# Kernel tuning notes

Hardware: AMD Instinct MI355X
Metric: run time of the kernel (lower is better)

Reference implementation:

```python
import jax, jax.numpy as jnp
import numpy as np

N, E = 16000, 256000
IN_DIM, HID, OUT_DIM, NH = 128, 128, 128, 16
HD = OUT_DIM // NH  # 8
EDGE_F, R_F = 4, 20
KV_IN = 2 * IN_DIM + EDGE_F + R_F  # 280
EPS = 1e-5
INV_SQRT_HD = float(1.0 / np.sqrt(HD))


def _ln(x, g, b):
    mu = jnp.mean(x, -1, keepdims=True)
    var = jnp.mean(jnp.square(x - mu), -1, keepdims=True)
    return (x - mu) * jax.lax.rsqrt(var + EPS) * g + b


def _mlp(x, W1, b1, g, be, W2, b2):
    # Linear -> LayerNorm -> ReLU -> Linear (targetdiff-style 2-layer MLP)
    hdn = jax.nn.relu(_ln(x @ W1 + b1, g, be))
    return hdn @ W2 + b2


def setup_inputs() -> dict:
    key = jax.random.key(0)
    k = jax.random.split(key, 16)
    s = 0.02
    f32 = jnp.float32
    return {
        "h": jax.random.normal(k[0], (N, IN_DIM), f32),
        "rel_x": jax.random.normal(k[1], (E, 3), f32),
        "r_feat": jax.random.uniform(k[2], (E, R_F), f32),
        "edge_feat": jax.random.normal(k[3], (E, EDGE_F), f32),
        "edge_index": jax.random.randint(k[4], (2, E), 0, N),
        # xk MLP: KV_IN -> HID -> OUT_DIM
        "xk_W1": jax.random.normal(k[5], (KV_IN, HID), f32) * s,
        "xk_b1": jnp.zeros((HID,), f32),
        "xk_g": jnp.ones((HID,), f32),
        "xk_be": jnp.zeros((HID,), f32),
        "xk_W2": jax.random.normal(k[6], (HID, OUT_DIM), f32) * s,
        "xk_b2": jnp.zeros((OUT_DIM,), f32),
        # xv MLP: KV_IN -> HID -> NH
        "xv_W1": jax.random.normal(k[7], (KV_IN, HID), f32) * s,
        "xv_b1": jnp.zeros((HID,), f32),
        "xv_g": jnp.ones((HID,), f32),
        "xv_be": jnp.zeros((HID,), f32),
        "xv_W2": jax.random.normal(k[8], (HID, NH), f32) * s,
        "xv_b2": jnp.zeros((NH,), f32),
        # xq MLP: IN_DIM -> HID -> OUT_DIM
        "xq_W1": jax.random.normal(k[9], (IN_DIM, HID), f32) * s,
        "xq_b1": jnp.zeros((HID,), f32),
        "xq_g": jnp.ones((HID,), f32),
        "xq_be": jnp.zeros((HID,), f32),
        "xq_W2": jax.random.normal(k[10], (HID, OUT_DIM), f32) * s,
        "xq_b2": jnp.zeros((OUT_DIM,), f32),
        # ew_net: Linear(R_F, 1) + sigmoid
        "ew_W": jax.random.normal(k[11], (R_F, 1), f32) * s,
        "ew_b": jnp.zeros((1,), f32),
    }


def reference(h, rel_x, r_feat, edge_feat, edge_index,
              xk_W1, xk_b1, xk_g, xk_be, xk_W2, xk_b2,
              xv_W1, xv_b1, xv_g, xv_be, xv_W2, xv_b2,
              xq_W1, xq_b1, xq_g, xq_be, xq_W2, xq_b2,
              ew_W, ew_b):
    n = h.shape[0]
    src, dst = edge_index[0], edge_index[1]
    hi, hj = h[dst], h[src]                                    # [E, IN_DIM] each
    kv_input = jnp.concatenate([edge_feat, r_feat, hi, hj], -1)  # [E, KV_IN]
    k = _mlp(kv_input, xk_W1, xk_b1, xk_g, xk_be, xk_W2, xk_b2).reshape(-1, NH, HD)
    v = _mlp(kv_input, xv_W1, xv_b1, xv_g, xv_be, xv_W2, xv_b2)  # [E, NH]
    e_w = jax.nn.sigmoid(r_feat @ ew_W + ew_b)                   # [E, 1]
    v = v * e_w
    v = v[:, :, None] * rel_x[:, None, :]                        # [E, NH, 3]
    q = _mlp(h, xq_W1, xq_b1, xq_g, xq_be, xq_W2, xq_b2).reshape(-1, NH, HD)
    scores = jnp.sum(q[dst] * k, -1) * INV_SQRT_HD               # [E, NH]
    # scatter_softmax over dst groups (numerically stable)
    smax = jax.lax.stop_gradient(jax.ops.segment_max(scores, dst, num_segments=n))
    ex = jnp.exp(scores - smax[dst])
    denom = jax.ops.segment_sum(ex, dst, num_segments=n)
    alpha = ex / denom[dst]                                      # [E, NH]
    m = alpha[:, :, None] * v                                    # [E, NH, 3]
    out = jax.ops.segment_sum(m, dst, num_segments=n)            # [N, NH, 3]
    return out.mean(1)                                           # [N, 3]
```

## Files before the change

kernel.cpp:

```cpp
#include <hip/hip_runtime.h>
#include <math.h>

#define NN 16000
#define NE 256000
#define INV_SQRT_HD 0.35355339059327373f
#define LN_EPS 1e-5f

typedef __attribute__((ext_vector_type(8))) short bf16x8;
typedef __attribute__((ext_vector_type(4))) float f32x4;

__device__ inline unsigned short f2bf(float x) {
    unsigned u = __float_as_uint(x);
    unsigned r = ((u >> 16) & 1u) + 0x7FFFu;
    return (unsigned short)((u + r) >> 16);
}

__global__ __launch_bounds__(256) void prep_kernel(
    const float* __restrict__ h,
    const float* __restrict__ r_feat,
    const float* __restrict__ edge_feat,
    const float* __restrict__ ewW, const float* __restrict__ ewB,
    const float* __restrict__ kW1, const float* __restrict__ vW1,
    const float* __restrict__ kW2, const float* __restrict__ vW2,
    const float* __restrict__ qW1, const float* __restrict__ qW2,
    unsigned short* __restrict__ h_bf, unsigned short* __restrict__ feats_bf,
    float* __restrict__ ew_pre,
    unsigned short* __restrict__ w1p, unsigned short* __restrict__ w2p,
    unsigned short* __restrict__ w1q, unsigned short* __restrict__ w2q)
{
    const int b = blockIdx.x, t = threadIdx.x;
    if (b < 1000) {
        const int gid = b * 256 + t;
        const float4* hp = (const float4*)(h + (size_t)gid * 8);
        float4 a = hp[0], c = hp[1];
        ushort4 u0, u1;
        u0.x = f2bf(a.x); u0.y = f2bf(a.y); u0.z = f2bf(a.z); u0.w = f2bf(a.w);
        u1.x = f2bf(c.x); u1.y = f2bf(c.y); u1.z = f2bf(c.z); u1.w = f2bf(c.w);
        *(ushort4*)(h_bf + (size_t)gid * 8) = u0;
        *(ushort4*)(h_bf + (size_t)gid * 8 + 4) = u1;
    } else if (b < 2000) {
        const int e = (b - 1000) * 256 + t;
        float4 ef = *(const float4*)(edge_feat + (size_t)e * 4);
        float rf[20];
        #pragma unroll
        for (int i = 0; i < 5; ++i)
            *(float4*)&rf[i * 4] = *(const float4*)(r_feat + (size_t)e * 20 + i * 4);
        float z = ewB[0];
        #pragma unroll
        for (int i = 0; i < 20; ++i) z = fmaf(rf[i], ewW[i], z);
        ew_pre[e] = (1.f / (1.f + expf(-z))) * (1.f / 16.f);
        unsigned short fb[32];
        fb[0] = f2bf(ef.x); fb[1] = f2bf(ef.y); fb[2] = f2bf(ef.z); fb[3] = f2bf(ef.w);
        #pragma unroll
        for (int i = 0; i < 20; ++i) fb[4 + i] = f2bf(rf[i]);
        #pragma unroll
        for (int i = 24; i < 32; ++i) fb[i] = 0;
        #pragma unroll
        for (int i = 0; i < 4; ++i)
            *(int4*)(feats_bf + (size_t)e * 32 + i * 8) = *(int4*)&fb[i * 8];
    } else {
        const int idx = (b - 2000) * 256 + t;
        if (idx < 73728) {
            int j = idx & 7, l = (idx >> 3) & 63, mtc = (idx >> 9) & 15, s = idx >> 13;
            int kp = s * 32 + (l >> 4) * 8 + j;
            int col = mtc * 16 + (l & 15);
            float v = 0.f;
            int row = (kp < 24) ? kp : ((kp >= 32) ? (kp - 8) : -1);
            if (row >= 0) v = (col < 128) ? kW1[(size_t)row * 128 + col]
                                          : vW1[(size_t)row * 128 + col - 128];
            w1p[idx] = f2bf(v);
        } else if (idx < 92160) {
            int i2 = idx - 73728;
            int j = i2 & 7, l = (i2 >> 3) & 63, sc = i2 >> 9;
            int ct = sc % 9, s2 = sc / 9;
            int k = s2 * 32 + (l >> 4) * 8 + j;
            float v = (ct < 8) ? kW2[(size_t)k * 128 + ct * 16 + (l & 15)]
                               : vW2[(size_t)k * 16 + (l & 15)];
            w2p[i2] = f2bf(v);
        } else if (idx < 108544) {
            int i3 = idx - 92160;
            int j = i3 & 7, l = (i3 >> 3) & 63, mt = (i3 >> 9) & 7, s = i3 >> 12;
            int k = s * 32 + (l >> 4) * 8 + j;
            w1q[i3] = f2bf(qW1[(size_t)k * 128 + mt * 16 + (l & 15)]);
        } else if (idx < 124928) {
            int i4 = idx - 108544;
            int j = i4 & 7, l = (i4 >> 3) & 63, mt = (i4 >> 9) & 7, s = i4 >> 12;
            int k = s * 32 + (l >> 4) * 8 + j;
            w2q[i4] = f2bf(qW2[(size_t)k * 128 + mt * 16 + (l & 15)]);
        }
    }
}

__global__ __launch_bounds__(256, 4) void qmlp_kernel(
    const unsigned short* __restrict__ h_bf,
    const float* __restrict__ B1, const float* __restrict__ G,
    const float* __restrict__ BE, const float* __restrict__ B2,
    const unsigned short* __restrict__ w1q, const unsigned short* __restrict__ w2q,
    float* __restrict__ qout)
{
    __shared__ __align__(16) unsigned char hsq[8192];
    __shared__ float2 lnb[4][32];
    __shared__ float  gb1[128];
    __shared__ float2 gbe[128];
    __shared__ float  gb2[128];

    const int t = threadIdx.x;
    const int nb = blockIdx.x * 32;
    const int wc = t >> 6, l = t & 63, lrow = l & 15, lgrp = l >> 4;

    if (t < 128) { gb1[t] = B1[t]; gbe[t] = make_float2(G[t], BE[t]); gb2[t] = B2[t]; }

    unsigned offN[2];
    #pragma unroll
    for (int nt = 0; nt < 2; ++nt)
        offN[nt] = (unsigned)(nb + nt * 16 + lrow) * 128 + lgrp * 8;
    __syncthreads();

    f32x4 acc1[2][2];
    #pragma unroll
    for (int mt = 0; mt < 2; ++mt) {
        const int cb = wc * 32 + mt * 16 + lgrp * 4;
        #pragma unroll
        for (int nt = 0; nt < 2; ++nt) {
            acc1[mt][nt][0] = gb1[cb];     acc1[mt][nt][1] = gb1[cb + 1];
            acc1[mt][nt][2] = gb1[cb + 2]; acc1[mt][nt][3] = gb1[cb + 3];
        }
    }
    {
        auto ldA = [&](int s, bf16x8* dst) {
            #pragma unroll
            for (int mt = 0; mt < 2; ++mt)
                dst[mt] = *(const bf16x8*)(w1q + (size_t)((s * 8 + wc * 2 + mt) * 64 + l) * 8);
        };
        auto ldB = [&](int s, bf16x8* dst) {
            #pragma unroll
            for (int nt = 0; nt < 2; ++nt)
                dst[nt] = *(const bf16x8*)(h_bf + offN[nt] + s * 32);
        };
        bf16x8 aB[2][2], bB[2][2];
        ldA(0, aB[0]); ldB(0, bB[0]);
        ldA(1, aB[1]); ldB(1, bB[1]);
        #pragma unroll
        for (int s = 0; s < 4; ++s) {
            const int c = s & 1;
            #pragma unroll
            for (int mt = 0; mt < 2; ++mt)
                #pragma unroll
                for (int nt = 0; nt < 2; ++nt)
                    acc1[mt][nt] = __builtin_amdgcn_mfma_f32_16x16x32_bf16(aB[c][mt], bB[c][nt], acc1[mt][nt], 0, 0, 0);
            if (s < 2) { ldA(s + 2, aB[c]); ldB(s + 2, bB[c]); }
        }
    }

    float2 myln[2];
    #pragma unroll
    for (int nt = 0; nt < 2; ++nt) {
        float p1 = 0.f, p2 = 0.f;
        #pragma unroll
        for (int mt = 0; mt < 2; ++mt)
            #pragma unroll
            for (int r = 0; r < 4; ++r) { float v = acc1[mt][nt][r]; p1 += v; p2 += v * v; }
        p1 += __shfl_xor(p1, 16); p2 += __shfl_xor(p2, 16);
        p1 += __shfl_xor(p1, 32); p2 += __shfl_xor(p2, 32);
        myln[nt] = make_float2(p1, p2);
        if (l < 16) lnb[wc][nt * 16 + l] = myln[nt];
    }
    __syncthreads();

    #pragma unroll
    for (int nt = 0; nt < 2; ++nt) {
        const int el = nt * 16 + lrow;
        float2 a0 = lnb[0][el], a1 = lnb[1][el], a2 = lnb[2][el], a3 = lnb[3][el];
        const float s1 = a0.x + a1.x + a2.x + a3.x;
        const float s2 = a0.y + a1.y + a2.y + a3.y;
        const float mu = s1 * (1.f / 128.f);
        const float rs = rsqrtf(s2 * (1.f / 128.f) - mu * mu + LN_EPS);
        #pragma unroll
        for (int mt = 0; mt < 2; ++mt) {
            const int cb = wc * 32 + mt * 16 + lgrp * 4;
            const float2 g0 = gbe[cb], g1 = gbe[cb+1], g2 = gbe[cb+2], g3 = gbe[cb+3];
            ushort4 u;
            u.x = f2bf(fmaxf((acc1[mt][nt][0] - mu) * rs * g0.x + g0.y, 0.f));
            u.y = f2bf(fmaxf((acc1[mt][nt][1] - mu) * rs * g1.x + g1.y, 0.f));
            u.z = f2bf(fmaxf((acc1[mt][nt][2] - mu) * rs * g2.x + g2.y, 0.f));
            u.w = f2bf(fmaxf((acc1[mt][nt][3] - mu) * rs * g3.x + g3.y, 0.f));
            *(ushort4*)(hsq + ((cb >> 3) * 32 + el) * 16 + (lgrp & 1) * 8) = u;
        }
    }
    __syncthreads();

    f32x4 acc2[2][2];
    #pragma unroll
    for (int km = 0; km < 2; ++km) {
        const int c2 = (wc * 2 + km) * 16 + lgrp * 4;
        #pragma unroll
        for (int nt = 0; nt < 2; ++nt) {
            acc2[km][nt][0] = gb2[c2];     acc2[km][nt][1] = gb2[c2 + 1];
            acc2[km][nt][2] = gb2[c2 + 2]; acc2[km][nt][3] = gb2[c2 + 3];
        }
    }
    {
        bf16x8 a0C = *(const bf16x8*)(w2q + (size_t)((wc * 2) * 64 + l) * 8);
        bf16x8 a1C = *(const bf16x8*)(w2q + (size_t)((wc * 2 + 1) * 64 + l) * 8);
        #pragma unroll
        for (int s2 = 0; s2 < 4; ++s2) {
            bf16x8 a0N, a1N;
            if (s2 < 3) {
                a0N = *(const bf16x8*)(w2q + (size_t)(((s2+1) * 8 + wc * 2) * 64 + l) * 8);
                a1N = *(const bf16x8*)(w2q + (size_t)(((s2+1) * 8 + wc * 2 + 1) * 64 + l) * 8);
            }
            bf16x8 hb[2];
            #pragma unroll
            for (int nt = 0; nt < 2; ++nt)
                hb[nt] = *(const bf16x8*)(hsq + (((s2 * 4 + lgrp) * 32) + nt * 16 + lrow) * 16);
            #pragma unroll
            for (int nt = 0; nt < 2; ++nt) {
                acc2[0][nt] = __builtin_amdgcn_mfma_f32_16x16x32_bf16(a0C, hb[nt], acc2[0][nt], 0, 0, 0);
                acc2[1][nt] = __builtin_amdgcn_mfma_f32_16x16x32_bf16(a1C, hb[nt], acc2[1][nt], 0, 0, 0);
            }
            a0C = a0N; a1C = a1N;
        }
    }
    #pragma unroll
    for (int km = 0; km < 2; ++km) {
        const int c2 = (wc * 2 + km) * 16 + lgrp * 4;
        #pragma unroll
        for (int nt = 0; nt < 2; ++nt) {
            const int el = nt * 16 + lrow;
            float4 o;
            o.x = acc2[km][nt][0]; o.y = acc2[km][nt][1];
            o.z = acc2[km][nt][2]; o.w = acc2[km][nt][3];
            *(float4*)(qout + (size_t)(nb + el) * 128 + c2) = o;
        }
    }
}

__global__ __launch_bounds__(256, 4) void edge_kernel(
    const unsigned short* __restrict__ h_bf,
    const unsigned short* __restrict__ feats_bf,
    const int*   __restrict__ eidx,
    const float* __restrict__ ew_pre,
    const float* __restrict__ kB1, const float* __restrict__ kG, const float* __restrict__ kBE,
    const float* __restrict__ vB1, const float* __restrict__ vG, const float* __restrict__ vBE,
    const float* __restrict__ kB2, const float* __restrict__ vB2,
    const unsigned short* __restrict__ w1p, const unsigned short* __restrict__ w2p,
    const float* __restrict__ q,
    float* __restrict__ ex_out, float* __restrict__ vw_out, float* __restrict__ denom)
{
    __shared__ __align__(16) unsigned char hs[16384];
    __shared__ float2 lnb[4][32];
    __shared__ float  gb1[256];
    __shared__ float2 gbe[256];
    __shared__ float  gb2[144];
    __shared__ int    dst_sh[32];
    __shared__ float  ew_s[32];

    const int t = threadIdx.x;
    const int eb = blockIdx.x * 32;
    const int wc = t >> 6, l = t & 63, lrow = l & 15, lgrp = l >> 4;

    gb1[t] = (t < 128) ? kB1[t] : vB1[t - 128];
    gbe[t] = make_float2((t < 128) ? kG[t] : vG[t - 128],
                         (t < 128) ? kBE[t] : vBE[t - 128]);
    if (t < 144) gb2[t] = (t < 128) ? kB2[t] : vB2[t - 128];
    if (t < 32) {
        dst_sh[t] = eidx[NE + eb + t];
        ew_s[t]   = ew_pre[eb + t];
    }

    unsigned offF[2], offD[2], offS[2];
    #pragma unroll
    for (int nt = 0; nt < 2; ++nt) {
        const int e = eb + nt * 16 + lrow;
        offF[nt] = (unsigned)e * 32 + lgrp * 8;
        offD[nt] = (unsigned)eidx[NE + e] * 128 + lgrp * 8;
        offS[nt] = (unsigned)eidx[e] * 128 + lgrp * 8;
    }
    __syncthreads();

    f32x4 acc1[4][2];
    #pragma unroll
    for (int mt = 0; mt < 4; ++mt) {
        const int cb = wc * 64 + mt * 16 + lgrp * 4;
        #pragma unroll
        for (int nt = 0; nt < 2; ++nt) {
            acc1[mt][nt][0] = gb1[cb];     acc1[mt][nt][1] = gb1[cb + 1];
            acc1[mt][nt][2] = gb1[cb + 2]; acc1[mt][nt][3] = gb1[cb + 3];
        }
    }
    {
        auto ldA = [&](int s, bf16x8* dst) {
            #pragma unroll
            for (int mt = 0; mt < 4; ++mt)
                dst[mt] = *(const bf16x8*)(w1p + (size_t)((s * 16 + wc * 4 + mt) * 64 + l) * 8);
        };
        auto ldB = [&](int s, bf16x8* dst) {
            #pragma unroll
            for (int nt = 0; nt < 2; ++nt) {
                const unsigned short* p = (s == 0) ? (feats_bf + offF[nt])
                                        : (s <= 4) ? (h_bf + offD[nt] + (s - 1) * 32)
                                                   : (h_bf + offS[nt] + (s - 5) * 32);
                dst[nt] = *(const bf16x8*)p;
            }
        };
        bf16x8 aB[2][4], bB[2][2];
        ldA(0, aB[0]); ldB(0, bB[0]);
        ldA(1, aB[1]); ldB(1, bB[1]);
        #pragma unroll
        for (int s = 0; s < 9; ++s) {
            const int c = s & 1;
            #pragma unroll
            for (int mt = 0; mt < 4; ++mt)
                #pragma unroll
                for (int nt = 0; nt < 2; ++nt)
                    acc1[mt][nt] = __builtin_amdgcn_mfma_f32_16x16x32_bf16(aB[c][mt], bB[c][nt], acc1[mt][nt], 0, 0, 0);
            if (s < 7) { ldA(s + 2, aB[c]); ldB(s + 2, bB[c]); }
        }
    }

    float2 myln[2];
    #pragma unroll
    for (int nt = 0; nt < 2; ++nt) {
        float p1 = 0.f, p2 = 0.f;
        #pragma unroll
        for (int mt = 0; mt < 4; ++mt)
            #pragma unroll
            for (int r = 0; r < 4; ++r) { float v = acc1[mt][nt][r]; p1 += v; p2 += v * v; }
        p1 += __shfl_xor(p1, 16); p2 += __shfl_xor(p2, 16);
        p1 += __shfl_xor(p1, 32); p2 += __shfl_xor(p2, 32);
        myln[nt] = make_float2(p1, p2);
        if (l < 16) lnb[wc][nt * 16 + l] = myln[nt];
    }
    __syncthreads();

    #pragma unroll
    for (int nt = 0; nt < 2; ++nt) {
        const int el = nt * 16 + lrow;
        const float2 oth = lnb[wc ^ 1][el];
        const float s1 = myln[nt].x + oth.x, s2 = myln[nt].y + oth.y;
        const float mu = s1 * (1.f / 128.f);
        const float rs = rsqrtf(s2 * (1.f / 128.f) - mu * mu + LN_EPS);
        #pragma unroll
        for (int mt = 0; mt < 4; ++mt) {
            const int cb = wc * 64 + mt * 16 + lgrp * 4;
            const int region = cb >> 7, kc = cb & 127;
            const float2 g0 = gbe[cb], g1 = gbe[cb+1], g2 = gbe[cb+2], g3 = gbe[cb+3];
            ushort4 u;
            u.x = f2bf(fmaxf((acc1[mt][nt][0] - mu) * rs * g0.x + g0.y, 0.f));
            u.y = f2bf(fmaxf((acc1[mt][nt][1] - mu) * rs * g1.x + g1.y, 0.f));
            u.z = f2bf(fmaxf((acc1[mt][nt][2] - mu) * rs * g2.x + g2.y, 0.f));
            u.w = f2bf(fmaxf((acc1[mt][nt][3] - mu) * rs * g3.x + g3.y, 0.f));
            *(ushort4*)(hs + region * 8192 + ((kc >> 3) * 32 + el) * 16 + (lgrp & 1) * 8) = u;
        }
    }
    __syncthreads();

    f32x4 acc2[2][2], accv;
    #pragma unroll
    for (int km = 0; km < 2; ++km) {
        const int c0 = (wc * 2 + km) * 16 + lgrp * 4;
        #pragma unroll
        for (int nt = 0; nt < 2; ++nt) {
            acc2[km][nt][0] = gb2[c0];     acc2[km][nt][1] = gb2[c0 + 1];
            acc2[km][nt][2] = gb2[c0 + 2]; acc2[km][nt][3] = gb2[c0 + 3];
        }
    }
    const int vel = wc * 16 + lrow;
    {
        const int cv = 128 + lgrp * 4;
        accv[0] = gb2[cv]; accv[1] = gb2[cv+1]; accv[2] = gb2[cv+2]; accv[3] = gb2[cv+3];
    }
    {
        bf16x8 a0C = *(const bf16x8*)(w2p + (size_t)((wc * 2) * 64 + l) * 8);
        bf16x8 a1C = *(const bf16x8*)(w2p + (size_t)((wc * 2 + 1) * 64 + l) * 8);
        bf16x8 avC = *(const bf16x8*)(w2p + (size_t)(8 * 64 + l) * 8);
        #pragma unroll
        for (int s2 = 0; s2 < 4; ++s2) {
            bf16x8 a0N, a1N, avN;
            if (s2 < 3) {
                a0N = *(const bf16x8*)(w2p + (size_t)(((s2+1) * 9 + wc * 2) * 64 + l) * 8);
                a1N = *(const bf16x8*)(w2p + (size_t)(((s2+1) * 9 + wc * 2 + 1) * 64 + l) * 8);
                avN = *(const bf16x8*)(w2p + (size_t)(((s2+1) * 9 + 8) * 64 + l) * 8);
            }
            bf16x8 hb[2];
            #pragma unroll
            for (int nt = 0; nt < 2; ++nt)
                hb[nt] = *(const bf16x8*)(hs + ((s2 * 4 + lgrp) * 32 + nt * 16 + lrow) * 16);
            #pragma unroll
            for (int nt = 0; nt < 2; ++nt) {
                acc2[0][nt] = __builtin_amdgcn_mfma_f32_16x16x32_bf16(a0C, hb[nt], acc2[0][nt], 0, 0, 0);
                acc2[1][nt] = __builtin_amdgcn_mfma_f32_16x16x32_bf16(a1C, hb[nt], acc2[1][nt], 0, 0, 0);
            }
            if (wc < 2) {
                bf16x8 hv = *(const bf16x8*)(hs + 8192 + ((s2 * 4 + lgrp) * 32 + vel) * 16);
                accv = __builtin_amdgcn_mfma_f32_16x16x32_bf16(avC, hv, accv, 0, 0, 0);
            }
            a0C = a0N; a1C = a1N; avC = avN;
        }
    }

    if (wc < 2) {
        const float sc = ew_s[vel];
        float4 vo;
        vo.x = accv[0] * sc; vo.y = accv[1] * sc; vo.z = accv[2] * sc; vo.w = accv[3] * sc;
        *(float4*)(vw_out + (size_t)(eb + vel) * 16 + lgrp * 4) = vo;
    }

    #pragma unroll
    for (int km = 0; km < 2; ++km) {
        #pragma unroll
        for (int nt = 0; nt < 2; ++nt) {
            const int el = nt * 16 + lrow;
            const int c0 = (wc * 2 + km) * 16 + lgrp * 4;
            const int dst = dst_sh[el];
            const float4 qv = *(const float4*)(q + (size_t)dst * 128 + c0);
            float sp = acc2[km][nt][0] * qv.x + acc2[km][nt][1] * qv.y
                     + acc2[km][nt][2] * qv.z + acc2[km][nt][3] * qv.w;
            sp += __shfl_xor(sp, 16);
            if ((l & 16) == 0) {
                const float exv = expf(sp * INV_SQRT_HD);
                const int hh = (wc * 2 + km) * 2 + (lgrp >> 1);
                ex_out[(size_t)(eb + el) * 16 + hh] = exv;
                atomicAdd(&denom[(size_t)dst * 16 + hh], exv);
            }
        }
    }
}

__global__ __launch_bounds__(256) void finalize_kernel(
    const int* __restrict__ eidx, const float* __restrict__ relx,
    const float* __restrict__ exb, const float* __restrict__ vwb,
    const float* __restrict__ den, float* __restrict__ out)
{
    const int e = blockIdx.x * 256 + threadIdx.x;
    const int dst = eidx[NE + e];
    const float4* ex4 = (const float4*)(exb + (size_t)e*16);
    const float4* vw4 = (const float4*)(vwb + (size_t)e*16);
    const float4* dn4 = (const float4*)(den + (size_t)dst*16);
    float s = 0.f;
    #pragma unroll
    for (int k = 0; k < 4; ++k) {
        float4 a = ex4[k], b = vw4[k], d = dn4[k];
        s += (a.x/d.x)*b.x + (a.y/d.y)*b.y + (a.z/d.z)*b.z + (a.w/d.w)*b.w;
    }
    float r0 = relx[(size_t)e*3+0], r1 = relx[(size_t)e*3+1], r2 = relx[(size_t)e*3+2];
    atomicAdd(&out[(size_t)dst*3+0], s*r0);
    atomicAdd(&out[(size_t)dst*3+1], s*r1);
    atomicAdd(&out[(size_t)dst*3+2], s*r2);
}

extern "C" void kernel_launch(void* const* d_in, const int* in_sizes, int n_in,
                              void* d_out, int out_size, void* d_ws, size_t ws_size,
                              hipStream_t stream) {
    const float* h         = (const float*)d_in[0];
    const float* rel_x     = (const float*)d_in[1];
    const float* r_feat    = (const float*)d_in[2];
    const float* edge_feat = (const float*)d_in[3];
    const int*   eidx      = (const int*)  d_in[4];
    const float* kW1 = (const float*)d_in[5];
    const float* kB1 = (const float*)d_in[6];
    const float* kG  = (const float*)d_in[7];
    const float* kBE = (const float*)d_in[8];
    const float* kW2 = (const float*)d_in[9];
    const float* kB2 = (const float*)d_in[10];
    const float* vW1 = (const float*)d_in[11];
    const float* vB1 = (const float*)d_in[12];
    const float* vG  = (const float*)d_in[13];
    const float* vBE = (const float*)d_in[14];
    const float* vW2 = (const float*)d_in[15];
    const float* vB2 = (const float*)d_in[16];
    const float* qW1 = (const float*)d_in[17];
    const float* qB1 = (const float*)d_in[18];
    const float* qG  = (const float*)d_in[19];
    const float* qBE = (const float*)d_in[20];
    const float* qW2 = (const float*)d_in[21];
    const float* qB2 = (const float*)d_in[22];
    const float* ewW = (const float*)d_in[23];
    const float* ewB = (const float*)d_in[24];

    float* ws   = (float*)d_ws;
    float* qbuf = ws;
    float* exb  = qbuf + (size_t)NN*128;
    float* vwb  = exb + (size_t)NE*16;
    float* den  = vwb + (size_t)NE*16;
    float* ewp  = den + (size_t)NN*16;
    unsigned short* w1p  = (unsigned short*)(ewp + (size_t)NE);
    unsigned short* w2p  = w1p + 73728;
    unsigned short* w1q  = w2p + 18432;
    unsigned short* w2q  = w1q + 16384;
    unsigned short* h_bf = w2q + 16384;
    unsigned short* feats_bf = h_bf + (size_t)NN*128;
    float* outf = (float*)d_out;

    hipMemsetAsync(den, 0, (size_t)NN*16*sizeof(float), stream);
    hipMemsetAsync(outf, 0, (size_t)NN*3*sizeof(float), stream);

    prep_kernel<<<2488, 256, 0, stream>>>(h, r_feat, edge_feat, ewW, ewB,
                                          kW1, vW1, kW2, vW2, qW1, qW2,
                                          h_bf, feats_bf, ewp, w1p, w2p, w1q, w2q);
    qmlp_kernel<<<NN/32, 256, 0, stream>>>(h_bf, qB1, qG, qBE, qB2, w1q, w2q, qbuf);
    edge_kernel<<<NE/32, 256, 0, stream>>>(h_bf, feats_bf, eidx, ewp,
                                           kB1, kG, kBE, vB1, vG, vBE,
                                           kB2, vB2, w1p, w2p, qbuf,
                                           exb, vwb, den);
    finalize_kernel<<<NE/256, 256, 0, stream>>>(eidx, rel_x, exb, vwb, den, outf);
}
```

Measured before the change: 274.7 us.

## Stage edge gather into LDS, prefetch q early, store q as bf16

```diff
diff --git a/kernel.cpp b/kernel.cpp
--- a/kernel.cpp
+++ b/kernel.cpp
@@ -13,6 +13,9 @@
     unsigned u = __float_as_uint(x);
     unsigned r = ((u >> 16) & 1u) + 0x7FFFu;
     return (unsigned short)((u + r) >> 16);
+}
+__device__ inline float bf2f(unsigned short u) {
+    return __uint_as_float(((unsigned)u) << 16);
 }
 
 __global__ __launch_bounds__(256) void prep_kernel(
@@ -96,7 +99,7 @@
     const float* __restrict__ B1, const float* __restrict__ G,
     const float* __restrict__ BE, const float* __restrict__ B2,
     const unsigned short* __restrict__ w1q, const unsigned short* __restrict__ w2q,
-    float* __restrict__ qout)
+    unsigned short* __restrict__ q_bf)
 {
     __shared__ __align__(16) unsigned char hsq[8192];
     __shared__ float2 lnb[4][32];
@@ -227,15 +230,15 @@
         #pragma unroll
         for (int nt = 0; nt < 2; ++nt) {
             const int el = nt * 16 + lrow;
-            float4 o;
-            o.x = acc2[km][nt][0]; o.y = acc2[km][nt][1];
-            o.z = acc2[km][nt][2]; o.w = acc2[km][nt][3];
-            *(float4*)(qout + (size_t)(nb + el) * 128 + c2) = o;
-        }
-    }
-}
-
-__global__ __launch_bounds__(256, 4) void edge_kernel(
+            ushort4 o;
+            o.x = f2bf(acc2[km][nt][0]); o.y = f2bf(acc2[km][nt][1]);
+            o.z = f2bf(acc2[km][nt][2]); o.w = f2bf(acc2[km][nt][3]);
+            *(ushort4*)(q_bf + (size_t)(nb + el) * 128 + c2) = o;
+        }
+    }
+}
+
+__global__ __launch_bounds__(256, 3) void edge_kernel(
     const unsigned short* __restrict__ h_bf,
     const unsigned short* __restrict__ feats_bf,
     const int*   __restrict__ eidx,
@@ -244,37 +247,55 @@
     const float* __restrict__ vB1, const float* __restrict__ vG, const float* __restrict__ vBE,
     const float* __restrict__ kB2, const float* __restrict__ vB2,
     const unsigned short* __restrict__ w1p, const unsigned short* __restrict__ w2p,
-    const float* __restrict__ q,
+    const unsigned short* __restrict__ q_bf,
     float* __restrict__ ex_out, float* __restrict__ vw_out, float* __restrict__ denom)
 {
+    __shared__ __align__(16) unsigned char xs[18432];
     __shared__ __align__(16) unsigned char hs[16384];
     __shared__ float2 lnb[4][32];
     __shared__ float  gb1[256];
     __shared__ float2 gbe[256];
     __shared__ float  gb2[144];
-    __shared__ int    dst_sh[32];
     __shared__ float  ew_s[32];
 
     const int t = threadIdx.x;
     const int eb = blockIdx.x * 32;
     const int wc = t >> 6, l = t & 63, lrow = l & 15, lgrp = l >> 4;
+
+    int4 stg[5];
+    #pragma unroll
+    for (int r = 0; r < 5; ++r) {
+        const int idx = r * 256 + t;
+        if (idx < 1152) {
+            const int c = idx >> 5, e_loc = idx & 31, e = eb + e_loc;
+            const unsigned short* p;
+            if (c < 4)       p = feats_bf + (size_t)e * 32 + c * 8;
+            else if (c < 20) p = h_bf + (size_t)eidx[NE + e] * 128 + (c - 4) * 8;
+            else             p = h_bf + (size_t)eidx[e] * 128 + (c - 20) * 8;
+            stg[r] = *(const int4*)p;
+        }
+    }
+
+    int dst01[2];
+    #pragma unroll
+    for (int nt = 0; nt < 2; ++nt) dst01[nt] = eidx[NE + eb + nt * 16 + lrow];
+    int2 qreg[2][2];
+    #pragma unroll
+    for (int km = 0; km < 2; ++km)
+        #pragma unroll
+        for (int nt = 0; nt < 2; ++nt)
+            qreg[km][nt] = *(const int2*)(q_bf + (size_t)dst01[nt] * 128 + (wc * 2 + km) * 16 + lgrp * 4);
 
     gb1[t] = (t < 128) ? kB1[t] : vB1[t - 128];
     gbe[t] = make_float2((t < 128) ? kG[t] : vG[t - 128],
                          (t < 128) ? kBE[t] : vBE[t - 128]);
     if (t < 144) gb2[t] = (t < 128) ? kB2[t] : vB2[t - 128];
-    if (t < 32) {
-        dst_sh[t] = eidx[NE + eb + t];
-        ew_s[t]   = ew_pre[eb + t];
-    }
-
-    unsigned offF[2], offD[2], offS[2];
-    #pragma unroll
-    for (int nt = 0; nt < 2; ++nt) {
-        const int e = eb + nt * 16 + lrow;
-        offF[nt] = (unsigned)e * 32 + lgrp * 8;
-        offD[nt] = (unsigned)eidx[NE + e] * 128 + lgrp * 8;
-        offS[nt] = (unsigned)eidx[e] * 128 + lgrp * 8;
+    if (t < 32) ew_s[t] = ew_pre[eb + t];
+
+    #pragma unroll
+    for (int r = 0; r < 5; ++r) {
+        const int idx = r * 256 + t;
+        if (idx < 1152) *(int4*)(xs + idx * 16) = stg[r];
     }
     __syncthreads();
 
@@ -296,12 +317,8 @@
         };
         auto ldB = [&](int s, bf16x8* dst) {
             #pragma unroll
-            for (int nt = 0; nt < 2; ++nt) {
-                const unsigned short* p = (s == 0) ? (feats_bf + offF[nt])
-                                        : (s <= 4) ? (h_bf + offD[nt] + (s - 1) * 32)
-                                                   : (h_bf + offS[nt] + (s - 5) * 32);
-                dst[nt] = *(const bf16x8*)p;
-            }
+            for (int nt = 0; nt < 2; ++nt)
+                dst[nt] = *(const bf16x8*)(xs + (((s * 4 + lgrp) * 32) + nt * 16 + lrow) * 16);
         };
         bf16x8 aB[2][4], bB[2][2];
         ldA(0, aB[0]); ldB(0, bB[0]);
@@ -411,17 +428,19 @@
         #pragma unroll
         for (int nt = 0; nt < 2; ++nt) {
             const int el = nt * 16 + lrow;
-            const int c0 = (wc * 2 + km) * 16 + lgrp * 4;
-            const int dst = dst_sh[el];
-            const float4 qv = *(const float4*)(q + (size_t)dst * 128 + c0);
-            float sp = acc2[km][nt][0] * qv.x + acc2[km][nt][1] * qv.y
-                     + acc2[km][nt][2] * qv.z + acc2[km][nt][3] * qv.w;
+            const int2 qv = qreg[km][nt];
+            const float q0 = bf2f((unsigned short)(qv.x & 0xffff));
+            const float q1 = bf2f((unsigned short)(((unsigned)qv.x) >> 16));
+            const float q2 = bf2f((unsigned short)(qv.y & 0xffff));
+            const float q3 = bf2f((unsigned short)(((unsigned)qv.y) >> 16));
+            float sp = acc2[km][nt][0] * q0 + acc2[km][nt][1] * q1
+                     + acc2[km][nt][2] * q2 + acc2[km][nt][3] * q3;
             sp += __shfl_xor(sp, 16);
             if ((l & 16) == 0) {
                 const float exv = expf(sp * INV_SQRT_HD);
                 const int hh = (wc * 2 + km) * 2 + (lgrp >> 1);
                 ex_out[(size_t)(eb + el) * 16 + hh] = exv;
-                atomicAdd(&denom[(size_t)dst * 16 + hh], exv);
+                atomicAdd(&denom[(size_t)dst01[nt] * 16 + hh], exv);
             }
         }
     }
@@ -490,6 +509,7 @@
     unsigned short* w2q  = w1q + 16384;
     unsigned short* h_bf = w2q + 16384;
     unsigned short* feats_bf = h_bf + (size_t)NN*128;
+    unsigned short* q_bf = (unsigned short*)qbuf;
     float* outf = (float*)d_out;
 
     hipMemsetAsync(den, 0, (size_t)NN*16*sizeof(float), stream);
@@ -498,10 +518,10 @@
     prep_kernel<<<2488, 256, 0, stream>>>(h, r_feat, edge_feat, ewW, ewB,
                                           kW1, vW1, kW2, vW2, qW1, qW2,
                                           h_bf, feats_bf, ewp, w1p, w2p, w1q, w2q);
-    qmlp_kernel<<<NN/32, 256, 0, stream>>>(h_bf, qB1, qG, qBE, qB2, w1q, w2q, qbuf);
+    qmlp_kernel<<<NN/32, 256, 0, stream>>>(h_bf, qB1, qG, qBE, qB2, w1q, w2q, q_bf);
     edge_kernel<<<NE/32, 256, 0, stream>>>(h_bf, feats_bf, eidx, ewp,
                                            kB1, kG, kBE, vB1, vG, vBE,
-                                           kB2, vB2, w1p, w2p, qbuf,
+                                           kB2, vB2, w1p, w2p, q_bf,
                                            exb, vwb, den);
     finalize_kernel<<<NE/256, 256, 0, stream>>>(eidx, rel_x, exb, vwb, den, outf);
 }
```

New measurement: 278.6 us, median of 5. About the same (+1.4%).
